# Optimization experiments

Measured on AMD Instinct MI355X. Metric: run time of the kernel, lower is better.

Reference implementation:

```python
import jax, jax.numpy as jnp
import numpy as np

NC, ND, B, K = 10000, 1000000, 8192, 64
EMB = 16
CH_DENSE, DEV_DENSE = 16, 20
CAT_MAX = [100, 4, 50, 200, 500, 1000, 300]  # lang, plat, os, country, carrier, brand, plat_os
H1, H2, ATTN_H = 64, 64, 84
IN1 = CH_DENSE + EMB        # 32  (channel dense + channel_id emb)
IN2 = DEV_DENSE + 7 * EMB   # 132 (device dense + 7 cat embs)


def setup_inputs() -> dict:
    key = jax.random.key(0)
    ks = jax.random.split(key, 32)
    def nrm(k, shape, s=0.05):
        return jax.random.normal(k, shape, dtype=jnp.float32) * s
    inp = {}
    inp["channel_dense"] = nrm(ks[0], (NC, CH_DENSE), 1.0)
    inp["device_dense"] = nrm(ks[1], (ND, DEV_DENSE), 1.0)
    inp["channel_id_emb"] = nrm(ks[2], (NC, EMB))
    names = ["lang_emb", "plat_emb", "os_emb", "country_emb", "carrier_emb", "brand_emb", "plat_os_emb"]
    for i, (n, m) in enumerate(zip(names, CAT_MAX)):
        inp[n] = nrm(ks[3 + i], (m, EMB))
    inp["W_agg"] = nrm(ks[10], (IN2, H2));  inp["b_agg"] = jnp.zeros((H2,), jnp.float32)
    inp["W_self"] = nrm(ks[11], (IN1, H1)); inp["b_self"] = jnp.zeros((H1,), jnp.float32)
    inp["W_attn"] = nrm(ks[12], (H2 + IN1, ATTN_H)); inp["b_attn"] = jnp.zeros((ATTN_H,), jnp.float32)
    inp["W_attn2"] = nrm(ks[13], (ATTN_H, 1)); inp["b_attn2"] = jnp.zeros((1,), jnp.float32)
    inp["channel_ids"] = jax.random.randint(ks[14], (NC,), 0, NC)
    cat_cols = [jax.random.randint(ks[15 + i], (ND,), 0, m) for i, m in enumerate(CAT_MAX)]
    inp["device_cat"] = jnp.stack(cat_cols, axis=1)  # [ND, 7]
    inp["vertices"] = jax.random.randint(ks[22], (B,), 0, NC)
    inp["bot_neibrs"] = jax.random.randint(ks[23], (B, K), 0, ND)
    inp["normal_neibrs"] = jax.random.randint(ks[24], (B, K), 0, ND)
    inp["bot_counts"] = jax.random.randint(ks[25], (B,), 1, K + 1)
    inp["normal_counts"] = jax.random.randint(ks[26], (B,), 1, K + 1)
    return inp


def reference(channel_dense, device_dense, channel_id_emb, lang_emb, plat_emb, os_emb,
              country_emb, carrier_emb, brand_emb, plat_os_emb,
              W_agg, b_agg, W_self, b_self, W_attn, b_attn, W_attn2, b_attn2,
              channel_ids, device_cat, vertices, bot_neibrs, normal_neibrs,
              bot_counts, normal_counts):
    cat_tables = [lang_emb, plat_emb, os_emb, country_emb, carrier_emb, brand_emb, plat_os_emb]
    # channel self features: dense cols + channel_id embedding  -> [B, IN1]
    ch_v = jnp.concatenate([channel_dense[vertices],
                            channel_id_emb[channel_ids[vertices]]], axis=1)

    def agg(neibrs, counts):
        # gather neighbor device features, embed categoricals, masked mean, linear (Mean_agg)
        dense = device_dense[neibrs]                                   # [B, K, DEV_DENSE]
        cats = device_cat[neibrs]                                      # [B, K, 7]
        embs = jnp.concatenate([t[cats[..., i]] for i, t in enumerate(cat_tables)], axis=-1)
        feats = jnp.concatenate([dense, embs], axis=-1)                # [B, K, IN2]
        mask = (jnp.arange(K)[None, :] < counts[:, None]).astype(feats.dtype)
        mean = jnp.sum(feats * mask[..., None], axis=1) / jnp.maximum(counts, 1).astype(feats.dtype)[:, None]
        return mean @ W_agg + b_agg                                    # [B, H2]

    bots = agg(bot_neibrs, bot_counts)
    normal = agg(normal_neibrs, normal_counts)

    def score(h):
        # attention MLP on concat(aggregated feats, channel self feats)
        return jax.nn.relu(jnp.concatenate([h, ch_v], axis=1) @ W_attn + b_attn) @ W_attn2 + b_attn2

    a = jax.nn.softmax(jnp.concatenate([score(bots), score(normal)], axis=1), axis=1)  # [B, 2]
    gcn = a[:, 0:1] * bots + a[:, 1:2] * normal                        # convex combination [B, H2]
    # Msg_out: relu(concat(agg_out, linear(self)))
    return jax.nn.relu(jnp.concatenate([gcn, ch_v @ W_self + b_self], axis=1))  # [B, H2+H1]
```

## Files before the change

### kernel.cpp

```cpp
#include <hip/hip_runtime.h>

#define BATCH 8192
#define KNB   64
#define EMB   16
#define CHD   16
#define DVD   20
#define H1    64
#define H2    64
#define AH    84
#define IN1   32
#define IN2   132

#define RB 32
#define VB 16

typedef float vf4 __attribute__((ext_vector_type(4)));

__global__ __launch_bounds__(256, 6) void gconv_gather(
    const float* __restrict__ device_dense,
    const float* __restrict__ t0, const float* __restrict__ t1,
    const float* __restrict__ t2, const float* __restrict__ t3,
    const float* __restrict__ t4, const float* __restrict__ t5,
    const float* __restrict__ t6,
    const int* __restrict__ device_cat,
    const int* __restrict__ bot_neibrs,
    const int* __restrict__ normal_neibrs,
    const int* __restrict__ bot_counts,
    const int* __restrict__ normal_counts,
    float* __restrict__ fsum_ws)
{
    const int t    = threadIdx.x;
    const int w    = t >> 6;
    const int L    = t & 63;
    const int kk   = L >> 5;
    const int slot = L & 31;
    const int item = blockIdx.x * 4 + w;
    const int v    = item >> 1;

    __shared__ alignas(16) float lds_tab[2464];
    __shared__ alignas(16) int   ofs[4][KNB][8];

    for (int i = t; i < 616; i += 256) {
        float4 vsrc;
        if (i < 400)      vsrc = ((const float4*)t0)[i];
        else if (i < 416) vsrc = ((const float4*)t1)[i - 400];
        else              vsrc = ((const float4*)t2)[i - 416];
        ((float4*)lds_tab)[i] = vsrc;
    }

    int cnt = (item & 1) ? normal_counts[v] : bot_counts[v];
    cnt = cnt < 1 ? 1 : (cnt > KNB ? KNB : cnt);
    cnt = __builtin_amdgcn_readfirstlane(cnt);

    {
        const int* nb = (item & 1) ? normal_neibrs : bot_neibrs;
        int n = 0;
        if (L < cnt) n = nb[v * KNB + L];
        const long cb = (long)n * 7;
        const int4 cA = *(const int4*)(device_cat + cb);
        const int4 cB = *(const int4*)(device_cat + cb + 3);
        *(int4*)&ofs[w][L][0] = make_int4(n * DVD, cA.x * EMB,
                                          1600 + cA.y * EMB, 1664 + cA.z * EMB);
        *(int4*)&ofs[w][L][4] = make_int4(cA.w * EMB, cB.y * EMB,
                                          cB.z * EMB, cB.w * EMB);
    }
    __syncthreads();

    const float* P = device_dense;
    int oIdx, col, feat;
    if (slot < 5)       { P = device_dense; oIdx = 0; col = 4 * slot;  feat = col; }
    else if (slot < 9)  { P = t3; oIdx = 4; col = 4 * (slot - 5);  feat = 68  + col; }
    else if (slot < 13) { P = t4; oIdx = 5; col = 4 * (slot - 9);  feat = 84  + col; }
    else if (slot < 17) { P = t5; oIdx = 6; col = 4 * (slot - 13); feat = 100 + col; }
    else if (slot < 21) { P = t6; oIdx = 7; col = 4 * (slot - 17); feat = 116 + col; }
    else if (slot < 25) { oIdx = 1; col = 4 * (slot - 21); feat = 20 + col; }
    else if (slot < 29) { oIdx = 3; col = 4 * (slot - 25); feat = 52 + col; }
    else                { oIdx = 2; col = 4 * (slot - 29); feat = 36 + col; }
    const bool isG = (slot < 21);

    vf4 acc  = {0.f, 0.f, 0.f, 0.f};
    vf4 acc2 = {0.f, 0.f, 0.f, 0.f};
    const int passes = (cnt + 1) >> 1;
    for (int pc = 0; pc < passes; pc += 8) {
        int o[8];
        #pragma unroll
        for (int j = 0; j < 8; ++j)
            o[j] = ofs[w][2 * (pc + j) + kk][oIdx];
        if (isG) {
            vf4 val[8];
            #pragma unroll
            for (int j = 0; j < 8; ++j) {
                const float* ap = P + o[j] + col;
                asm volatile("global_load_dwordx4 %0, %1, off"
                             : "=v"(val[j]) : "v"(ap) : "memory");
            }
            asm volatile("s_waitcnt vmcnt(0)" ::: "memory");
            __builtin_amdgcn_sched_barrier(0);
            #pragma unroll
            for (int j = 0; j < 8; ++j) {
                const float m = (2 * (pc + j) + kk < cnt) ? 1.f : 0.f;
                acc[0] = fmaf(m, val[j][0], acc[0]);
                acc[1] = fmaf(m, val[j][1], acc[1]);
                acc[2] = fmaf(m, val[j][2], acc[2]);
                acc[3] = fmaf(m, val[j][3], acc[3]);
            }
        } else {
            #pragma unroll
            for (int j = 0; j < 8; ++j) {
                const float m = (2 * (pc + j) + kk < cnt) ? 1.f : 0.f;
                const float4 lv = *(const float4*)&lds_tab[o[j] + col];
                acc[0] = fmaf(m, lv.x, acc[0]);
                acc[1] = fmaf(m, lv.y, acc[1]);
                acc[2] = fmaf(m, lv.z, acc[2]);
                acc[3] = fmaf(m, lv.w, acc[3]);
                if (slot == 29) {
                    const float4 l2 = *(const float4*)&lds_tab[o[j] + 12];
                    acc2[0] = fmaf(m, l2.x, acc2[0]);
                    acc2[1] = fmaf(m, l2.y, acc2[1]);
                    acc2[2] = fmaf(m, l2.z, acc2[2]);
                    acc2[3] = fmaf(m, l2.w, acc2[3]);
                }
            }
        }
    }

    acc[0] += __shfl_xor(acc[0], 32, 64);
    acc[1] += __shfl_xor(acc[1], 32, 64);
    acc[2] += __shfl_xor(acc[2], 32, 64);
    acc[3] += __shfl_xor(acc[3], 32, 64);
    if (slot == 29) {
        acc2[0] += __shfl_xor(acc2[0], 32, 64);
        acc2[1] += __shfl_xor(acc2[1], 32, 64);
        acc2[2] += __shfl_xor(acc2[2], 32, 64);
        acc2[3] += __shfl_xor(acc2[3], 32, 64);
    }

    if (L < 32)
        *(float4*)(fsum_ws + (size_t)item * IN2 + feat) =
            make_float4(acc[0], acc[1], acc[2], acc[3]);
    if (L == 29)
        *(float4*)(fsum_ws + (size_t)item * IN2 + 48) =
            make_float4(acc2[0], acc2[1], acc2[2], acc2[3]);
}

__global__ __launch_bounds__(256) void gconv_dense(
    const float* __restrict__ channel_dense,
    const float* __restrict__ channel_id_emb,
    const float* __restrict__ W_agg,  const float* __restrict__ b_agg,
    const float* __restrict__ W_self, const float* __restrict__ b_self,
    const float* __restrict__ W_attn, const float* __restrict__ b_attn,
    const float* __restrict__ W_attn2,
    const int* __restrict__ channel_ids,
    const int* __restrict__ vertices,
    const int* __restrict__ bot_counts,
    const int* __restrict__ normal_counts,
    const float* __restrict__ fsum_ws,
    float* __restrict__ out)
{
    const int blk = blockIdx.x;
    const int b0  = blk * RB;
    const int v0  = blk * VB;
    const int t   = threadIdx.x;

    __shared__ alignas(16) float fs[RB][IN2];
    __shared__ alignas(16) float chvs[VB][IN1];
    __shared__ alignas(16) float hs[RB][H2];
    __shared__ float u_lds[AH][RB + 1];
    __shared__ float sarr[RB];
    __shared__ float cinv[RB];

    for (int idx = t; idx < RB * IN2 / 4; idx += 256) {
        const float4 vv = *(const float4*)(fsum_ws + (size_t)b0 * IN2 + idx * 4);
        *(float4*)&((float*)fs)[idx * 4] = vv;
    }
    if (t < RB) {
        const int b = b0 + t;
        const int v = b >> 1;
        int c = (b & 1) ? normal_counts[v] : bot_counts[v];
        c = (c > KNB) ? KNB : ((c < 1) ? 1 : c);
        cinv[t] = 1.0f / (float)c;
    }
    if (t < 128) {
        const int vx = t >> 3, q = t & 7;
        const int vert = vertices[v0 + vx];
        const float* src = (q < 4)
            ? channel_dense  + (size_t)vert * CHD + q * 4
            : channel_id_emb + (size_t)channel_ids[vert] * EMB + (q - 4) * 4;
        *(float4*)&chvs[vx][q * 4] = *(const float4*)src;
    }
    __syncthreads();

    {
        const int w = t >> 6, lane = t & 63;
        const int r0 = w * 8;
        float acc[8] = {0.f, 0.f, 0.f, 0.f, 0.f, 0.f, 0.f, 0.f};
        #pragma unroll 4
        for (int f = 0; f < IN2; ++f) {
            const float wv = W_agg[f * H2 + lane];
            #pragma unroll
            for (int r = 0; r < 8; ++r)
                acc[r] = fmaf(fs[r0 + r][f], wv, acc[r]);
        }
        const float bb = b_agg[lane];
        #pragma unroll
        for (int r = 0; r < 8; ++r)
            hs[r0 + r][lane] = fmaf(acc[r], cinv[r0 + r], bb);
    }
    __syncthreads();

    if (t < 2 * AH) {
        const int rg = (t >= AH) ? 1 : 0;
        const int aa = t - AH * rg;
        const int r0 = rg * 16;
        float acc[16];
        #pragma unroll
        for (int r = 0; r < 16; ++r) acc[r] = 0.f;
        #pragma unroll 2
        for (int f = 0; f < H2; ++f) {
            const float wv = W_attn[f * AH + aa];
            #pragma unroll
            for (int r = 0; r < 16; ++r)
                acc[r] = fmaf(hs[r0 + r][f], wv, acc[r]);
        }
        #pragma unroll 2
        for (int f = 0; f < IN1; ++f) {
            const float wv = W_attn[(H2 + f) * AH + aa];
            #pragma unroll
            for (int r = 0; r < 16; ++r)
                acc[r] = fmaf(chvs[(r0 + r) >> 1][f], wv, acc[r]);
        }
        const float ba = b_attn[aa], w2 = W_attn2[aa];
        #pragma unroll
        for (int r = 0; r < 16; ++r)
            u_lds[aa][r0 + r] = fmaxf(acc[r] + ba, 0.f) * w2;
    }
    __syncthreads();

    if (t < RB) {
        float s = 0.f;
        #pragma unroll 4
        for (int aa = 0; aa < AH; ++aa) s += u_lds[aa][t];
        sarr[t] = s;
    }
    __syncthreads();

    {
        const int vl = t >> 4;
        const int c8 = (t & 15) * 8;
        const float s0 = sarr[2 * vl], s1 = sarr[2 * vl + 1];
        const float mm = fmaxf(s0, s1);
        const float e0 = __expf(s0 - mm), e1 = __expf(s1 - mm);
        const float rs = 1.0f / (e0 + e1);
        const float a0 = e0 * rs, a1 = e1 * rs;
        float o[8];
        if (c8 < H2) {
            #pragma unroll
            for (int c = 0; c < 8; ++c)
                o[c] = fmaxf(a0 * hs[2 * vl][c8 + c] + a1 * hs[2 * vl + 1][c8 + c], 0.f);
        } else {
            const int cs = c8 - H2;
            float accS[8];
            #pragma unroll
            for (int c = 0; c < 8; ++c) accS[c] = b_self[cs + c];
            #pragma unroll 4
            for (int f = 0; f < IN1; ++f) {
                const float xv = chvs[vl][f];
                const float4 wa = *(const float4*)(W_self + f * H1 + cs);
                const float4 wb = *(const float4*)(W_self + f * H1 + cs + 4);
                accS[0] = fmaf(xv, wa.x, accS[0]);
                accS[1] = fmaf(xv, wa.y, accS[1]);
                accS[2] = fmaf(xv, wa.z, accS[2]);
                accS[3] = fmaf(xv, wa.w, accS[3]);
                accS[4] = fmaf(xv, wb.x, accS[4]);
                accS[5] = fmaf(xv, wb.y, accS[5]);
                accS[6] = fmaf(xv, wb.z, accS[6]);
                accS[7] = fmaf(xv, wb.w, accS[7]);
            }
            #pragma unroll
            for (int c = 0; c < 8; ++c) o[c] = fmaxf(accS[c], 0.f);
        }
        float4* op = (float4*)(out + (size_t)(v0 + vl) * (H1 + H2) + c8);
        op[0] = make_float4(o[0], o[1], o[2], o[3]);
        op[1] = make_float4(o[4], o[5], o[6], o[7]);
    }
}

extern "C" void kernel_launch(void* const* d_in, const int* in_sizes, int n_in,
                              void* d_out, int out_size, void* d_ws, size_t ws_size,
                              hipStream_t stream) {
    const float* channel_dense  = (const float*)d_in[0];
    const float* device_dense   = (const float*)d_in[1];
    const float* channel_id_emb = (const float*)d_in[2];
    const float* lang_emb       = (const float*)d_in[3];
    const float* plat_emb       = (const float*)d_in[4];
    const float* os_emb         = (const float*)d_in[5];
    const float* country_emb    = (const float*)d_in[6];
    const float* carrier_emb    = (const float*)d_in[7];
    const float* brand_emb      = (const float*)d_in[8];
    const float* plat_os_emb    = (const float*)d_in[9];
    const float* W_agg          = (const float*)d_in[10];
    const float* b_agg          = (const float*)d_in[11];
    const float* W_self         = (const float*)d_in[12];
    const float* b_self         = (const float*)d_in[13];
    const float* W_attn         = (const float*)d_in[14];
    const float* b_attn         = (const float*)d_in[15];
    const float* W_attn2        = (const float*)d_in[16];
    const int* channel_ids   = (const int*)d_in[18];
    const int* device_cat    = (const int*)d_in[19];
    const int* vertices      = (const int*)d_in[20];
    const int* bot_neibrs    = (const int*)d_in[21];
    const int* normal_neibrs = (const int*)d_in[22];
    const int* bot_counts    = (const int*)d_in[23];
    const int* normal_counts = (const int*)d_in[24];

    float* fsum_ws = (float*)d_ws;
    float* out     = (float*)d_out;

    gconv_gather<<<dim3(2 * BATCH / 4), dim3(256), 0, stream>>>(
        device_dense, lang_emb, plat_emb, os_emb, country_emb, carrier_emb,
        brand_emb, plat_os_emb, device_cat, bot_neibrs, normal_neibrs,
        bot_counts, normal_counts, fsum_ws);

    gconv_dense<<<dim3(2 * BATCH / RB), dim3(256), 0, stream>>>(
        channel_dense, channel_id_emb, W_agg, b_agg, W_self, b_self,
        W_attn, b_attn, W_attn2, channel_ids, vertices,
        bot_counts, normal_counts, fsum_ws, out);
}
```

Measured before the change: 71.98 us.

## Stage all categorical embedding tables in LDS with 1024-thread blocks

Copies all seven categorical embedding tables (about 138KB) into shared memory, so that only the device_dense rows are still fetched by global gather and every embedding lookup reads LDS. Blocks grow to 1024 threads (16 items) to spread the table-load cost, and per-neighbor offsets are packed as 16-bit values to save LDS. The 138KB footprint allows at most one block per CU, which lowers occupancy and latency hiding for the global gathers. Each block also reloads the full tables from global memory, which adds traffic.

```diff
diff --git a/kernel.cpp b/kernel.cpp
--- a/kernel.cpp
+++ b/kernel.cpp
@@ -15,8 +15,19 @@
 #define VB 16
 
 typedef float vf4 __attribute__((ext_vector_type(4)));
-
-__global__ __launch_bounds__(256, 6) void gconv_gather(
+typedef unsigned short u16;
+typedef u16 u16x8 __attribute__((ext_vector_type(8)));
+
+#define TB_LANG    0
+#define TB_PLAT    1600
+#define TB_OS      1664
+#define TB_COUNTRY 2464
+#define TB_CARRIER 5664
+#define TB_BRAND   13664
+#define TB_PLATOS  29664
+#define TB_TOTAL   34464
+
+__global__ __launch_bounds__(1024, 4) void gconv_gather(
     const float* __restrict__ device_dense,
     const float* __restrict__ t0, const float* __restrict__ t1,
     const float* __restrict__ t2, const float* __restrict__ t3,
@@ -34,18 +45,23 @@
     const int L    = t & 63;
     const int kk   = L >> 5;
     const int slot = L & 31;
-    const int item = blockIdx.x * 4 + w;
+    const int item = blockIdx.x * 16 + w;
     const int v    = item >> 1;
 
-    __shared__ alignas(16) float lds_tab[2464];
-    __shared__ alignas(16) int   ofs[4][KNB][8];
-
-    for (int i = t; i < 616; i += 256) {
+    __shared__ alignas(16) float tab[TB_TOTAL];
+    __shared__ alignas(16) u16   o16[16][KNB][8];
+    __shared__ int               nds[16][KNB];
+
+    for (int i = t; i < 8616; i += 1024) {
         float4 vsrc;
-        if (i < 400)      vsrc = ((const float4*)t0)[i];
-        else if (i < 416) vsrc = ((const float4*)t1)[i - 400];
-        else              vsrc = ((const float4*)t2)[i - 416];
-        ((float4*)lds_tab)[i] = vsrc;
+        if (i < 400)       vsrc = ((const float4*)t0)[i];
+        else if (i < 416)  vsrc = ((const float4*)t1)[i - 400];
+        else if (i < 616)  vsrc = ((const float4*)t2)[i - 416];
+        else if (i < 1416) vsrc = ((const float4*)t3)[i - 616];
+        else if (i < 3416) vsrc = ((const float4*)t4)[i - 1416];
+        else if (i < 7416) vsrc = ((const float4*)t5)[i - 3416];
+        else               vsrc = ((const float4*)t6)[i - 7416];
+        ((float4*)tab)[i] = vsrc;
     }
 
     int cnt = (item & 1) ? normal_counts[v] : bot_counts[v];
@@ -59,38 +75,40 @@
         const long cb = (long)n * 7;
         const int4 cA = *(const int4*)(device_cat + cb);
         const int4 cB = *(const int4*)(device_cat + cb + 3);
-        *(int4*)&ofs[w][L][0] = make_int4(n * DVD, cA.x * EMB,
-                                          1600 + cA.y * EMB, 1664 + cA.z * EMB);
-        *(int4*)&ofs[w][L][4] = make_int4(cA.w * EMB, cB.y * EMB,
-                                          cB.z * EMB, cB.w * EMB);
-    }
-    __syncthreads();
-
-    const float* P = device_dense;
-    int oIdx, col, feat;
-    if (slot < 5)       { P = device_dense; oIdx = 0; col = 4 * slot;  feat = col; }
-    else if (slot < 9)  { P = t3; oIdx = 4; col = 4 * (slot - 5);  feat = 68  + col; }
-    else if (slot < 13) { P = t4; oIdx = 5; col = 4 * (slot - 9);  feat = 84  + col; }
-    else if (slot < 17) { P = t5; oIdx = 6; col = 4 * (slot - 13); feat = 100 + col; }
-    else if (slot < 21) { P = t6; oIdx = 7; col = 4 * (slot - 17); feat = 116 + col; }
-    else if (slot < 25) { oIdx = 1; col = 4 * (slot - 21); feat = 20 + col; }
-    else if (slot < 29) { oIdx = 3; col = 4 * (slot - 25); feat = 52 + col; }
-    else                { oIdx = 2; col = 4 * (slot - 29); feat = 36 + col; }
-    const bool isG = (slot < 21);
+        nds[w][L] = n * DVD;
+        u16x8 pk;
+        pk[0] = (u16)(cA.x * EMB); pk[1] = (u16)(cA.y * EMB);
+        pk[2] = (u16)(cA.z * EMB); pk[3] = (u16)(cA.w * EMB);
+        pk[4] = (u16)(cB.y * EMB); pk[5] = (u16)(cB.z * EMB);
+        pk[6] = (u16)(cB.w * EMB); pk[7] = 0;
+        *(u16x8*)&o16[w][L][0] = pk;
+    }
+    __syncthreads();
+
+    int base = 0, idx = 0, col = 0, feat = 0;
+    const bool isG = (slot < 5);
+    if (slot < 5)       { col = 4 * slot;        feat = col; }
+    else if (slot < 9)  { base = TB_LANG;    idx = 0; col = 4 * (slot - 5);  feat = 20  + col; }
+    else if (slot < 13) { base = TB_OS;      idx = 2; col = 4 * (slot - 9);  feat = 52  + col; }
+    else if (slot < 17) { base = TB_COUNTRY; idx = 3; col = 4 * (slot - 13); feat = 68  + col; }
+    else if (slot < 21) { base = TB_CARRIER; idx = 4; col = 4 * (slot - 17); feat = 84  + col; }
+    else if (slot < 25) { base = TB_BRAND;   idx = 5; col = 4 * (slot - 21); feat = 100 + col; }
+    else if (slot < 29) { base = TB_PLATOS;  idx = 6; col = 4 * (slot - 25); feat = 116 + col; }
+    else                { base = TB_PLAT;    idx = 1; col = 4 * (slot - 29); feat = 36  + col; }
 
     vf4 acc  = {0.f, 0.f, 0.f, 0.f};
     vf4 acc2 = {0.f, 0.f, 0.f, 0.f};
     const int passes = (cnt + 1) >> 1;
     for (int pc = 0; pc < passes; pc += 8) {
-        int o[8];
-        #pragma unroll
-        for (int j = 0; j < 8; ++j)
-            o[j] = ofs[w][2 * (pc + j) + kk][oIdx];
         if (isG) {
+            int o[8];
+            #pragma unroll
+            for (int j = 0; j < 8; ++j)
+                o[j] = nds[w][2 * (pc + j) + kk];
             vf4 val[8];
             #pragma unroll
             for (int j = 0; j < 8; ++j) {
-                const float* ap = P + o[j] + col;
+                const float* ap = device_dense + o[j] + col;
                 asm volatile("global_load_dwordx4 %0, %1, off"
                              : "=v"(val[j]) : "v"(ap) : "memory");
             }
@@ -107,14 +125,16 @@
         } else {
             #pragma unroll
             for (int j = 0; j < 8; ++j) {
-                const float m = (2 * (pc + j) + kk < cnt) ? 1.f : 0.f;
-                const float4 lv = *(const float4*)&lds_tab[o[j] + col];
+                const int k = 2 * (pc + j) + kk;
+                const float m = (k < cnt) ? 1.f : 0.f;
+                const int row = o16[w][k][idx];
+                const float4 lv = *(const float4*)&tab[base + row + col];
                 acc[0] = fmaf(m, lv.x, acc[0]);
                 acc[1] = fmaf(m, lv.y, acc[1]);
                 acc[2] = fmaf(m, lv.z, acc[2]);
                 acc[3] = fmaf(m, lv.w, acc[3]);
                 if (slot == 29) {
-                    const float4 l2 = *(const float4*)&lds_tab[o[j] + 12];
+                    const float4 l2 = *(const float4*)&tab[base + row + 12];
                     acc2[0] = fmaf(m, l2.x, acc2[0]);
                     acc2[1] = fmaf(m, l2.y, acc2[1]);
                     acc2[2] = fmaf(m, l2.z, acc2[2]);
@@ -142,6 +162,8 @@
         *(float4*)(fsum_ws + (size_t)item * IN2 + 48) =
             make_float4(acc2[0], acc2[1], acc2[2], acc2[3]);
 }
+#undef TB_PLAT
+#define TB_PLAT 1600
 
 __global__ __launch_bounds__(256) void gconv_dense(
     const float* __restrict__ channel_dense,
@@ -316,7 +338,7 @@
     float* fsum_ws = (float*)d_ws;
     float* out     = (float*)d_out;
 
-    gconv_gather<<<dim3(2 * BATCH / 4), dim3(256), 0, stream>>>(
+    gconv_gather<<<dim3(2 * BATCH / 16), dim3(1024), 0, stream>>>(
         device_dense, lang_emb, plat_emb, os_emb, country_emb, carrier_emb,
         brand_emb, plat_os_emb, device_cat, bot_neibrs, normal_neibrs,
         bot_counts, normal_counts, fsum_ws);
```

Result: slower. 101.1 us (+40.5%).
